# Kernel optimization log

Hardware: AMD Instinct MI355X
Metric: run time of the kernel (lower is better)

## Reference

```python
import jax, jax.numpy as jnp
import numpy as np

N_NODES = 100000
N_EDGES = 1600000
D_FEAT = 64
LATENT = 64
N_CLASSES = 16
NEG_SLOPE = 0.01  # flax nn.leaky_relu default negative_slope


def setup_inputs() -> dict:
    key = jax.random.key(0)
    ks = jax.random.split(key, 5)
    nodes = jax.random.normal(ks[0], (N_NODES, D_FEAT), dtype=jnp.float32)
    senders = jax.random.randint(ks[1], (N_EDGES,), 0, N_NODES)
    receivers = jax.random.randint(ks[2], (N_EDGES,), 0, N_NODES)
    # learned params (flax Dense: y = x @ kernel + bias)
    W0 = jax.random.normal(ks[3], (D_FEAT, LATENT), dtype=jnp.float32) / jnp.sqrt(D_FEAT)
    b0 = jnp.zeros((LATENT,), jnp.float32)
    W1 = jax.random.normal(ks[4], (LATENT, N_CLASSES), dtype=jnp.float32) / jnp.sqrt(LATENT)
    b1 = jnp.zeros((N_CLASSES,), jnp.float32)
    return {"nodes": nodes, "senders": senders, "receivers": receivers,
            "W0": W0, "b0": b0, "W1": W1, "b1": b1}


def _gcn_forward(nodes, W0, b0, W1, b1, senders, receivers):
    n = nodes.shape[0]
    ones = jnp.ones_like(senders, dtype=nodes.dtype)
    deg_s = jax.ops.segment_sum(ones, senders, n)    # out-degree of each node as sender
    deg_r = jax.ops.segment_sum(ones, receivers, n)  # in-degree of each node as receiver

    # Layer 1: GraphConvolution(Dense(latent), symmetric_normalization=True)
    h = nodes @ W0 + b0                                                  # [N, latent]
    h = h * jax.lax.rsqrt(jnp.maximum(deg_s, 1.0))[:, None]
    h = jax.ops.segment_sum(h[senders], receivers, n)                    # gather-scatter over edges
    h = h * jax.lax.rsqrt(jnp.maximum(deg_r, 1.0))[:, None]
    h = jnp.where(h >= 0, h, NEG_SLOPE * h)                              # leaky_relu

    # Layer 2: GraphConvolution(Dense(classes)+sigmoid, symmetric_normalization=False)
    z = jax.nn.sigmoid(h @ W1 + b1)                                      # [N, classes]
    out = jax.ops.segment_sum(z[senders], receivers, n)                  # unnormalized aggregation
    return out


def reference(nodes, senders, receivers, W0, b0, W1, b1):
    return _gcn_forward(nodes, W0, b0, W1, b1, senders, receivers)
```

## Files before the change

### kernel.cpp

```cpp
#include <hip/hip_runtime.h>
#include <hip/hip_bf16.h>

#define NN 100000
#define NE 1600000
#define D 64
#define C 16
#define NEG_SLOPE 0.01f
#define MCAP 64

#define NRG 8
#define RGW 12500
#define RWORDS 3125
#define NSR 64
#define EPSR 25000
#define B_RH (NSR * NRG)

#define NRANGE 8
#define RW 12544
#define WPR 3136
#define NSLICE 64
#define EPS 25000
#define B_HS (NRANGE * NSLICE)

#define B_GEMM 6250

typedef unsigned int u32;
typedef unsigned short u16;

__device__ __forceinline__ float bf2f(u32 u) { return __uint_as_float(u << 16); }
__device__ __forceinline__ u16 f2bf(float f) {
    __hip_bfloat16 b = __float2bfloat16(f);
    return *reinterpret_cast<u16*>(&b);
}

__global__ __launch_bounds__(256) void kA(
        const int* __restrict__ senders, const int* __restrict__ receivers,
        const float* __restrict__ nodes, const float* __restrict__ W0,
        const float* __restrict__ b0,
        u32* __restrict__ part_r, u32* __restrict__ part_s, u16* __restrict__ h) {
    __shared__ u32 smh[WPR];
    int bid = blockIdx.x, t = threadIdx.x;

    if (bid < B_RH) {
        int slice = bid >> 3, range = bid & 7;
        int lo = range * RGW;
        for (int i = t; i < RWORDS; i += 256) smh[i] = 0u;
        __syncthreads();
        const int* __restrict__ rp = receivers + slice * EPSR;
        for (int i = 4 * t; i < EPSR; i += 1024) {
            int4 v = *(const int4*)(rp + i);
            int r0 = v.x - lo, r1 = v.y - lo, r2 = v.z - lo, r3 = v.w - lo;
            if ((u32)r0 < (u32)RGW) atomicAdd(&smh[r0 >> 2], 1u << ((r0 & 3) * 8));
            if ((u32)r1 < (u32)RGW) atomicAdd(&smh[r1 >> 2], 1u << ((r1 & 3) * 8));
            if ((u32)r2 < (u32)RGW) atomicAdd(&smh[r2 >> 2], 1u << ((r2 & 3) * 8));
            if ((u32)r3 < (u32)RGW) atomicAdd(&smh[r3 >> 2], 1u << ((r3 & 3) * 8));
        }
        __syncthreads();
        u32* __restrict__ dst = part_r + ((size_t)slice * NRG + range) * RWORDS;
        for (int i = t; i < RWORDS; i += 256) dst[i] = smh[i];
    } else if (bid < B_RH + B_HS) {
        int hb = bid - B_RH;
        int rr = hb & 7, sl = hb >> 3;
        int lo = rr * RW;
        for (int i = t; i < WPR; i += 256) smh[i] = 0u;
        __syncthreads();
        const int* __restrict__ sp = senders + sl * EPS;
        for (int i = 4 * t; i < EPS; i += 1024) {
            int4 v = *(const int4*)(sp + i);
            int s0 = v.x - lo, s1 = v.y - lo, s2 = v.z - lo, s3 = v.w - lo;
            if ((u32)s0 < (u32)RW) atomicAdd(&smh[s0 >> 2], 1u << ((s0 & 3) * 8));
            if ((u32)s1 < (u32)RW) atomicAdd(&smh[s1 >> 2], 1u << ((s1 & 3) * 8));
            if ((u32)s2 < (u32)RW) atomicAdd(&smh[s2 >> 2], 1u << ((s2 & 3) * 8));
            if ((u32)s3 < (u32)RW) atomicAdd(&smh[s3 >> 2], 1u << ((s3 & 3) * 8));
        }
        __syncthreads();
        u32* __restrict__ dst = part_s + (size_t)hb * WPR;
        for (int i = t; i < WPR; i += 256) dst[i] = smh[i];
    } else {
        int wv = (bid - B_RH - B_HS) * 4 + (t >> 6);
        int lane = t & 63;
        int nsub = lane >> 4, q = lane & 15;
        int node = wv * 4 + nsub;
        const float* __restrict__ row = nodes + (size_t)node * D;
        float4 acc = ((const float4*)b0)[q];
#pragma unroll 16
        for (int k = 0; k < D; ++k) {
            float rk = row[k];
            float4 w4 = ((const float4*)(W0 + k * D))[q];
            acc.x = fmaf(rk, w4.x, acc.x);
            acc.y = fmaf(rk, w4.y, acc.y);
            acc.z = fmaf(rk, w4.z, acc.z);
            acc.w = fmaf(rk, w4.w, acc.w);
        }
        uint2 pk;
        pk.x = (u32)f2bf(acc.x) | ((u32)f2bf(acc.y) << 16);
        pk.y = (u32)f2bf(acc.z) | ((u32)f2bf(acc.w) << 16);
        *(uint2*)(h + (size_t)node * D + q * 4) = pk;
    }
}

__global__ __launch_bounds__(256) void kSc(u32* __restrict__ part_r,
                                           const u32* __restrict__ part_s,
                                           int* __restrict__ cnt_r,
                                           float* __restrict__ rnorm_s) {
    int bid = blockIdx.x, t = threadIdx.x;
    if (bid < 98) {
        int tid = bid * 256 + t;
        if (tid < NRG * RWORDS) {
            int range = tid / RWORDS, w = tid - range * RWORDS;
            u32* __restrict__ base = part_r + (size_t)range * RWORDS + w;
            u32 s0 = 0, s1 = 0, s2 = 0, s3 = 0;
            for (int sl = 0; sl < NSR; ++sl) {
                u32* p = base + (size_t)sl * (NRG * RWORDS);
                u32 v = *p;
                *p = s0 | (s1 << 8) | (s2 << 16) | (s3 << 24);
                s0 += v & 0xffu;
                s1 += (v >> 8) & 0xffu;
                s2 += (v >> 16) & 0xffu;
                s3 += (v >> 24) & 0xffu;
            }
            int node = range * RGW + w * 4;
            int4 cv; cv.x = (int)s0; cv.y = (int)s1; cv.z = (int)s2; cv.w = (int)s3;
            *(int4*)(cnt_r + node) = cv;
        }
    } else {
        int tid = (bid - 98) * 256 + t;
        if (tid < NRANGE * WPR) {
            int rr = tid / WPR;
            int w = tid - rr * WPR;
            const u32* __restrict__ p = part_s + (size_t)rr * WPR + w;
            u32 acc0 = 0, acc1 = 0;
#pragma unroll 8
            for (int sl = 0; sl < NSLICE; ++sl) {
                u32 v = p[(size_t)(sl * 8) * WPR];
                acc0 += v & 0x00FF00FFu;
                acc1 += (v >> 8) & 0x00FF00FFu;
            }
            int node = rr * RW + w * 4;
            u32 c0 = acc0 & 0xFFFFu, c1 = acc1 & 0xFFFFu, c2 = acc0 >> 16, c3 = acc1 >> 16;
            if (node + 3 < NN) {
                float4 o;
                o.x = rsqrtf((float)(c0 > 1u ? c0 : 1u));
                o.y = rsqrtf((float)(c1 > 1u ? c1 : 1u));
                o.z = rsqrtf((float)(c2 > 1u ? c2 : 1u));
                o.w = rsqrtf((float)(c3 > 1u ? c3 : 1u));
                *(float4*)(rnorm_s + node) = o;
            } else {
                u32 cc[4] = {c0, c1, c2, c3};
                for (int k = 0; k < 4; ++k)
                    if (node + k < NN)
                        rnorm_s[node + k] = rsqrtf((float)(cc[k] > 1u ? cc[k] : 1u));
            }
        }
    }
}

__global__ __launch_bounds__(256) void kF(
        const int* __restrict__ senders, const int* __restrict__ receivers,
        const u32* __restrict__ part_r,
        int* __restrict__ bucket) {
    __shared__ u32 smh[RWORDS];
    int bid = blockIdx.x, t = threadIdx.x;
    int slice = bid >> 3, range = bid & 7;
    int lo = range * RGW;
    const u32* __restrict__ pre = part_r + ((size_t)slice * NRG + range) * RWORDS;
    for (int i = t; i < RWORDS; i += 256) smh[i] = pre[i];
    __syncthreads();
    const int* __restrict__ rp = receivers + slice * EPSR;
    const int* __restrict__ sp = senders + slice * EPSR;
    for (int i = 4 * t; i < EPSR; i += 1024) {
        int4 rv = *(const int4*)(rp + i);
        int rl;
        rl = rv.x - lo;
        if ((u32)rl < (u32)RGW) {
            int w = rl >> 2, sh = (rl & 3) * 8;
            u32 old = atomicAdd(&smh[w], 1u << sh);
            int slot = (int)((old >> sh) & 0xffu);
            if (slot < MCAP) bucket[(lo + rl) * MCAP + slot] = sp[i];
        }
        rl = rv.y - lo;
        if ((u32)rl < (u32)RGW) {
            int w = rl >> 2, sh = (rl & 3) * 8;
            u32 old = atomicAdd(&smh[w], 1u << sh);
            int slot = (int)((old >> sh) & 0xffu);
            if (slot < MCAP) bucket[(lo + rl) * MCAP + slot] = sp[i + 1];
        }
        rl = rv.z - lo;
        if ((u32)rl < (u32)RGW) {
            int w = rl >> 2, sh = (rl & 3) * 8;
            u32 old = atomicAdd(&smh[w], 1u << sh);
            int slot = (int)((old >> sh) & 0xffu);
            if (slot < MCAP) bucket[(lo + rl) * MCAP + slot] = sp[i + 2];
        }
        rl = rv.w - lo;
        if ((u32)rl < (u32)RGW) {
            int w = rl >> 2, sh = (rl & 3) * 8;
            u32 old = atomicAdd(&smh[w], 1u << sh);
            int slot = (int)((old >> sh) & 0xffu);
            if (slot < MCAP) bucket[(lo + rl) * MCAP + slot] = sp[i + 3];
        }
    }
}

__global__ __launch_bounds__(256) void kB(
        const int* __restrict__ cnt_r, const int* __restrict__ bucket,
        const float* __restrict__ rnorm_s, const u16* __restrict__ h,
        const float* __restrict__ W1, const float* __restrict__ b1,
        u16* __restrict__ z) {
    __shared__ float sm[4][64];
    int wid = threadIdx.x >> 6, lane = threadIdx.x & 63;
    int node = blockIdx.x * 4 + wid;
    int deg = cnt_r[node];
    if (deg > MCAP) deg = MCAP;
    const int* __restrict__ row = bucket + node * MCAP;

    int my = 0; float rq = 0.f;
    if (lane < deg) {
        my = row[lane];
        rq = rnorm_s[my];
    }
    int qtr = lane >> 4, ql = lane & 15;
    float a0 = 0.f, a1 = 0.f, a2 = 0.f, a3 = 0.f;
    for (int j = 0; j < deg; j += 4) {
        int ei = j + qtr;
        int src = __shfl(my, ei, 64);
        float rs = __shfl(rq, ei, 64);
        uint2 w2 = *(const uint2*)(h + (size_t)src * D + ql * 4);
        if (ei < deg) {
            a0 = fmaf(rs, bf2f(w2.x & 0xffffu), a0);
            a1 = fmaf(rs, bf2f(w2.x >> 16),     a1);
            a2 = fmaf(rs, bf2f(w2.y & 0xffffu), a2);
            a3 = fmaf(rs, bf2f(w2.y >> 16),     a3);
        }
    }
    a0 += __shfl_xor(a0, 16, 64); a0 += __shfl_xor(a0, 32, 64);
    a1 += __shfl_xor(a1, 16, 64); a1 += __shfl_xor(a1, 32, 64);
    a2 += __shfl_xor(a2, 16, 64); a2 += __shfl_xor(a2, 32, 64);
    a3 += __shfl_xor(a3, 16, 64); a3 += __shfl_xor(a3, 32, 64);
    if (qtr == 0) {
        float rn = rsqrtf((float)(deg > 1 ? deg : 1));
        float v0 = a0 * rn; v0 = (v0 >= 0.f) ? v0 : NEG_SLOPE * v0;
        float v1 = a1 * rn; v1 = (v1 >= 0.f) ? v1 : NEG_SLOPE * v1;
        float v2 = a2 * rn; v2 = (v2 >= 0.f) ? v2 : NEG_SLOPE * v2;
        float v3 = a3 * rn; v3 = (v3 >= 0.f) ? v3 : NEG_SLOPE * v3;
        sm[wid][ql * 4 + 0] = v0;
        sm[wid][ql * 4 + 1] = v1;
        sm[wid][ql * 4 + 2] = v2;
        sm[wid][ql * 4 + 3] = v3;
    }
    asm volatile("s_waitcnt lgkmcnt(0)" ::: "memory");

    int c = lane & 15, q = lane >> 4;
    float p = 0.f;
#pragma unroll
    for (int i = 0; i < 16; ++i)
        p = fmaf(sm[wid][q * 16 + i], W1[(q * 16 + i) * C + c], p);
    p += __shfl_xor(p, 16, 64);
    p += __shfl_xor(p, 32, 64);
    if (lane < 16) {
        float zc = 1.f / (1.f + expf(-(p + b1[c])));
        z[(size_t)node * C + c] = f2bf(zc);
    }
}

__global__ __launch_bounds__(256) void kC(
        const int* __restrict__ cnt_r, const int* __restrict__ bucket,
        const u16* __restrict__ z, float* __restrict__ out) {
    int t = threadIdx.x;
    int lane = t & 63;
    int qtr = lane >> 4, ql = lane & 15;
    int node = blockIdx.x * 16 + (t >> 6) * 4 + qtr;
    int deg = cnt_r[node];
    if (deg > MCAP) deg = MCAP;
    const int* __restrict__ row = bucket + node * MCAP;

    int g2 = ql >> 2, p = ql & 3;
    float a0 = 0.f, a1 = 0.f, a2 = 0.f, a3 = 0.f;
    for (int base = 0; base < deg; base += 16) {
        int nb = deg - base; if (nb > 16) nb = 16;
        int my = (ql < nb) ? row[base + ql] : 0;
        for (int j = 0; j < nb; j += 4) {
            int ei = j + g2;
            int src = __shfl(my, (lane & 48) | ei, 64);
            uint2 w2 = *(const uint2*)(z + (size_t)src * C + p * 4);
            if (ei < nb) {
                a0 += bf2f(w2.x & 0xffffu);
                a1 += bf2f(w2.x >> 16);
                a2 += bf2f(w2.y & 0xffffu);
                a3 += bf2f(w2.y >> 16);
            }
        }
    }
    a0 += __shfl_xor(a0, 4, 64); a0 += __shfl_xor(a0, 8, 64);
    a1 += __shfl_xor(a1, 4, 64); a1 += __shfl_xor(a1, 8, 64);
    a2 += __shfl_xor(a2, 4, 64); a2 += __shfl_xor(a2, 8, 64);
    a3 += __shfl_xor(a3, 4, 64); a3 += __shfl_xor(a3, 8, 64);
    if (g2 == 0) {
        float4 o; o.x = a0; o.y = a1; o.z = a2; o.w = a3;
        *(float4*)(out + (size_t)node * C + p * 4) = o;
    }
}

extern "C" void kernel_launch(void* const* d_in, const int* in_sizes, int n_in,
                              void* d_out, int out_size, void* d_ws, size_t ws_size,
                              hipStream_t stream) {
    const float* nodes     = (const float*)d_in[0];
    const int*   senders   = (const int*)d_in[1];
    const int*   receivers = (const int*)d_in[2];
    const float* W0        = (const float*)d_in[3];
    const float* b0        = (const float*)d_in[4];
    const float* W1        = (const float*)d_in[5];
    const float* b1        = (const float*)d_in[6];
    float* out = (float*)d_out;

    char* wsb = (char*)d_ws;
    u32*   part_r  = (u32*)wsb;
    u32*   part_s  = (u32*)(wsb + 6400000);
    int*   cnt_r   = (int*)(wsb + 12822528);
    float* rnorm_s = (float*)(wsb + 13222528);
    int*   bucket  = (int*)(wsb + 13622528);
    u16*   h       = (u16*)(wsb + 39222528);
    u16*   z       = (u16*)(wsb + 52022528);

    kA<<<B_RH + B_HS + B_GEMM, 256, 0, stream>>>(senders, receivers, nodes, W0, b0,
                                                 part_r, part_s, h);
    kSc<<<196, 256, 0, stream>>>(part_r, part_s, cnt_r, rnorm_s);
    kF<<<B_RH, 256, 0, stream>>>(senders, receivers, part_r, bucket);
    kB<<<25000, 256, 0, stream>>>(cnt_r, bucket, rnorm_s, h, W1, b1, z);
    kC<<<6250, 256, 0, stream>>>(cnt_r, bucket, z, out);
}
```

Measured before the change: 278.2 us.

## Halve histogram ranges and software-pipeline gathers in aggregation kernels

The degree histograms now split nodes into 4 ranges instead of 8, with larger shared-memory tables. This halves the number of passes each block makes over the edge slices. In kB, each wave loads the whole bucket row unconditionally and prefetches the next neighbor row of h while accumulating the current one. kC also reads bucket entries unconditionally and clamps invalid indices. The changes trade more LDS per block and reads of uninitialized bucket slots, guarded by range clamping, for fewer redundant edge scans and more memory-level parallelism.

Measured after the change: 263.1 us. -5.5%, faster.

```diff
diff --git a/kernel.cpp b/kernel.cpp
--- a/kernel.cpp
+++ b/kernel.cpp
@@ -8,19 +8,18 @@
 #define NEG_SLOPE 0.01f
 #define MCAP 64
 
-#define NRG 8
-#define RGW 12500
-#define RWORDS 3125
+#define NRG 4
+#define RGW 25000
+#define RWORDS 6250
 #define NSR 64
 #define EPSR 25000
-#define B_RH (NSR * NRG)
-
-#define NRANGE 8
-#define RW 12544
-#define WPR 3136
+#define B_RH 256
+
+#define RW 25088
+#define WPR 6272
 #define NSLICE 64
 #define EPS 25000
-#define B_HS (NRANGE * NSLICE)
+#define B_HS 256
 
 #define B_GEMM 6250
 
@@ -42,7 +41,7 @@
     int bid = blockIdx.x, t = threadIdx.x;
 
     if (bid < B_RH) {
-        int slice = bid >> 3, range = bid & 7;
+        int range = bid & 3, slice = bid >> 2;
         int lo = range * RGW;
         for (int i = t; i < RWORDS; i += 256) smh[i] = 0u;
         __syncthreads();
@@ -56,11 +55,11 @@
             if ((u32)r3 < (u32)RGW) atomicAdd(&smh[r3 >> 2], 1u << ((r3 & 3) * 8));
         }
         __syncthreads();
-        u32* __restrict__ dst = part_r + ((size_t)slice * NRG + range) * RWORDS;
+        u32* __restrict__ dst = part_r + (size_t)bid * RWORDS;
         for (int i = t; i < RWORDS; i += 256) dst[i] = smh[i];
     } else if (bid < B_RH + B_HS) {
         int hb = bid - B_RH;
-        int rr = hb & 7, sl = hb >> 3;
+        int rr = hb & 3, sl = hb >> 2;
         int lo = rr * RW;
         for (int i = t; i < WPR; i += 256) smh[i] = 0u;
         __syncthreads();
@@ -125,14 +124,14 @@
         }
     } else {
         int tid = (bid - 98) * 256 + t;
-        if (tid < NRANGE * WPR) {
+        if (tid < NRG * WPR) {
             int rr = tid / WPR;
             int w = tid - rr * WPR;
             const u32* __restrict__ p = part_s + (size_t)rr * WPR + w;
             u32 acc0 = 0, acc1 = 0;
 #pragma unroll 8
             for (int sl = 0; sl < NSLICE; ++sl) {
-                u32 v = p[(size_t)(sl * 8) * WPR];
+                u32 v = p[(size_t)(sl * 4) * WPR];
                 acc0 += v & 0x00FF00FFu;
                 acc1 += (v >> 8) & 0x00FF00FFu;
             }
@@ -161,9 +160,9 @@
         int* __restrict__ bucket) {
     __shared__ u32 smh[RWORDS];
     int bid = blockIdx.x, t = threadIdx.x;
-    int slice = bid >> 3, range = bid & 7;
+    int range = bid & 3, slice = bid >> 2;
     int lo = range * RGW;
-    const u32* __restrict__ pre = part_r + ((size_t)slice * NRG + range) * RWORDS;
+    const u32* __restrict__ pre = part_r + (size_t)bid * RWORDS;
     for (int i = t; i < RWORDS; i += 256) smh[i] = pre[i];
     __syncthreads();
     const int* __restrict__ rp = receivers + slice * EPSR;
@@ -210,28 +209,31 @@
     __shared__ float sm[4][64];
     int wid = threadIdx.x >> 6, lane = threadIdx.x & 63;
     int node = blockIdx.x * 4 + wid;
+    const int* __restrict__ row = bucket + node * MCAP;
+
+    int raw = row[lane];
+    int my = ((u32)raw < (u32)NN) ? raw : 0;
+    float rq = rnorm_s[my];
     int deg = cnt_r[node];
     if (deg > MCAP) deg = MCAP;
-    const int* __restrict__ row = bucket + node * MCAP;
-
-    int my = 0; float rq = 0.f;
-    if (lane < deg) {
-        my = row[lane];
-        rq = rnorm_s[my];
-    }
+
     int qtr = lane >> 4, ql = lane & 15;
     float a0 = 0.f, a1 = 0.f, a2 = 0.f, a3 = 0.f;
+    int src = __shfl(my, qtr, 64);
+    float rs = __shfl(rq, qtr, 64);
+    uint2 w2 = *(const uint2*)(h + (size_t)src * D + ql * 4);
     for (int j = 0; j < deg; j += 4) {
-        int ei = j + qtr;
-        int src = __shfl(my, ei, 64);
-        float rs = __shfl(rq, ei, 64);
-        uint2 w2 = *(const uint2*)(h + (size_t)src * D + ql * 4);
-        if (ei < deg) {
+        int eiN = (j + 4 + qtr) & 63;
+        int srcN = __shfl(my, eiN, 64);
+        float rsN = __shfl(rq, eiN, 64);
+        uint2 wN = *(const uint2*)(h + (size_t)srcN * D + ql * 4);
+        if (j + qtr < deg) {
             a0 = fmaf(rs, bf2f(w2.x & 0xffffu), a0);
             a1 = fmaf(rs, bf2f(w2.x >> 16),     a1);
             a2 = fmaf(rs, bf2f(w2.y & 0xffffu), a2);
             a3 = fmaf(rs, bf2f(w2.y >> 16),     a3);
         }
+        w2 = wN; rs = rsN;
     }
     a0 += __shfl_xor(a0, 16, 64); a0 += __shfl_xor(a0, 32, 64);
     a1 += __shfl_xor(a1, 16, 64); a1 += __shfl_xor(a1, 32, 64);
@@ -278,7 +280,8 @@
     float a0 = 0.f, a1 = 0.f, a2 = 0.f, a3 = 0.f;
     for (int base = 0; base < deg; base += 16) {
         int nb = deg - base; if (nb > 16) nb = 16;
-        int my = (ql < nb) ? row[base + ql] : 0;
+        int raw = row[base + ql];
+        int my = ((u32)raw < (u32)NN) ? raw : 0;
         for (int j = 0; j < nb; j += 4) {
             int ei = j + g2;
             int src = __shfl(my, (lane & 48) | ei, 64);
```
